# Performance work log

Hardware: AMD Instinct MI355X
Metric: run time of the kernel (lower is better)

Reference implementation:

```python
import jax, jax.numpy as jnp
import numpy as np

EMBED_DIM = 768
SCALE = float(np.sqrt(EMBED_DIM / 9.0))


def setup_inputs() -> dict:
    key = jax.random.key(0)
    ks = jax.random.split(key, 7)
    D = EMBED_DIM
    s = 1.0 / np.sqrt(D)
    x = jax.random.normal(ks[0], (8, 2048, D), dtype=jnp.float32)
    Wq = jax.random.uniform(ks[1], (D, D), jnp.float32, -s, s)
    bq = jax.random.uniform(ks[2], (D,), jnp.float32, -s, s)
    Wk = jax.random.uniform(ks[3], (D, D), jnp.float32, -s, s)
    bk = jax.random.uniform(ks[4], (D,), jnp.float32, -s, s)
    Wv = jax.random.uniform(ks[5], (D, D), jnp.float32, -s, s)
    bv = jax.random.uniform(ks[6], (D,), jnp.float32, -s, s)
    return {"x": x, "Wq": Wq, "bq": bq, "Wk": Wk, "bk": bk, "Wv": Wv, "bv": bv}


def reference(x, Wq, bq, Wk, bk, Wv, bv):
    # nn.Linear: y = x @ W^T + b
    Q = jnp.einsum('bnd,ed->bne', x, Wq) + bq
    K = jnp.einsum('bnd,ed->bne', x, Wk) + bk
    V = jnp.einsum('bnd,ed->bne', x, Wv) + bv
    scores = jnp.einsum('bqd,bkd->bqk', Q, K) / SCALE  # [B, Nq, Nk]
    # NOTE: softmax over the QUERY axis (dim=-2), per the original module
    weights = jax.nn.softmax(scores, axis=-2)
    out = jnp.einsum('bqk,bkd->bqd', weights, V)
    return out + x
```

## Files before the change

### kernel.cpp

```cpp
#include <hip/hip_runtime.h>
#include <stdint.h>

#define B_ 8
#define N_ 2048
#define D_ 768

typedef unsigned short u16;
typedef unsigned int u32;
typedef __attribute__((ext_vector_type(8))) short bf16x8;
typedef __attribute__((ext_vector_type(8))) unsigned short u16x8;
typedef __attribute__((ext_vector_type(4))) float f32x4;

static constexpr float INV_SCALE = 0.10825317547305482f;

__device__ __forceinline__ u16 f2bf(float f) {
  union { float f; unsigned u; } v; v.f = f;
  return (u16)((v.u + 0x7FFFu + ((v.u >> 16) & 1u)) >> 16);
}
__device__ __forceinline__ float bf2f(u16 h) {
  union { unsigned u; float f; } v; v.u = ((unsigned)h) << 16;
  return v.f;
}
__device__ __forceinline__ f32x4 mfma16(bf16x8 a, bf16x8 b, f32x4 c) {
  return __builtin_amdgcn_mfma_f32_16x16x32_bf16(a, b, c, 0, 0, 0);
}
__device__ __forceinline__ void gl_lds16(const u16* g, u16* l) {
  __builtin_amdgcn_global_load_lds(
      (const __attribute__((address_space(1))) u32*)g,
      (__attribute__((address_space(3))) u32*)l, 16, 0, 0);
}

__global__ __launch_bounds__(256) void cast_kernel(
    const float* __restrict__ x, const float* __restrict__ wq,
    const float* __restrict__ wk, const float* __restrict__ wv,
    u16* __restrict__ xb, u16* __restrict__ wqb,
    u16* __restrict__ wkb, u16* __restrict__ wvb) {
  const long NX = (long)B_ * N_ * D_;
  const long NW = (long)D_ * D_;
  long i = ((long)blockIdx.x * 256 + threadIdx.x) * 8;
  const float* src; u16* dst; long off;
  if (i < NX) { src = x; dst = xb; off = i; }
  else {
    long j = i - NX;
    int seg = (int)(j / NW);
    off = j - (long)seg * NW;
    src = seg == 0 ? wq : (seg == 1 ? wk : wv);
    dst = seg == 0 ? wqb : (seg == 1 ? wkb : wvb);
  }
  float4 a = *(const float4*)(src + off);
  float4 b = *(const float4*)(src + off + 4);
  u16x8 o;
  o[0]=f2bf(a.x); o[1]=f2bf(a.y); o[2]=f2bf(a.z); o[3]=f2bf(a.w);
  o[4]=f2bf(b.x); o[5]=f2bf(b.y); o[6]=f2bf(b.z); o[7]=f2bf(b.w);
  *(u16x8*)(dst + off) = o;
}

template<int KSTEPS>
__device__ __forceinline__ void gemm_main(
    const u16* __restrict__ Ag, long lda,
    const u16* __restrict__ Bg, long ldb,
    f32x4 (&acc)[8][4]) {
  __shared__ u16 A0[4096], A1[4096], A2[4096];
  __shared__ u16 B0[8192], B1[8192], B2[8192];
  const int t_ = threadIdx.x, l = t_ & 63, w = t_ >> 6;
  const int lr = l & 15;
  const int srow = l >> 2;
  const int scol = (((l & 3) ^ ((l >> 3) & 3)) * 8);
  const int wc = w * 64;
  const int rslot = (((l >> 4) ^ ((lr >> 1) & 3)) * 8);

  auto STAGE = [&](u16* As, u16* Bs, int kt) {
    const int kofs = kt * 32;
    #pragma unroll
    for (int c = 0; c < 6; ++c) {
      int ch = w * 6 + c;
      if (ch < 8)
        gl_lds16(Ag + (long)(ch * 16 + srow) * lda + kofs + scol, As + ch * 512);
      else
        gl_lds16(Bg + (long)((ch - 8) * 16 + srow) * ldb + kofs + scol,
                 Bs + (ch - 8) * 512);
    }
  };

#define PH(AS, BS, VM, DOSTAGE, ST)                                \
  {                                                                \
    asm volatile("s_waitcnt vmcnt(" #VM ")" ::: "memory");         \
    __builtin_amdgcn_s_barrier();                                  \
    asm volatile("" ::: "memory");                                 \
    bf16x8 a[8], bb[4];                                            \
    _Pragma("unroll")                                              \
    for (int mf = 0; mf < 8; ++mf)                                 \
      a[mf] = *(const bf16x8*)(AS + (mf * 16 + lr) * 32 + rslot);  \
    _Pragma("unroll")                                              \
    for (int nf = 0; nf < 4; ++nf)                                 \
      bb[nf] = *(const bf16x8*)(BS + (wc + nf * 16 + lr) * 32 + rslot); \
    __builtin_amdgcn_s_setprio(1);                                 \
    _Pragma("unroll")                                              \
    for (int mf = 0; mf < 8; ++mf)                                 \
      _Pragma("unroll")                                            \
      for (int nf = 0; nf < 4; ++nf)                               \
        acc[mf][nf] = mfma16(a[mf], bb[nf], acc[mf][nf]);          \
    __builtin_amdgcn_s_setprio(0);                                 \
    asm volatile("" ::: "memory");                                 \
    __builtin_amdgcn_s_barrier();                                  \
    if (DOSTAGE) STAGE(AS, BS, ST);                                \
  }

  STAGE(A0, B0, 0);
  STAGE(A1, B1, 1);
  STAGE(A2, B2, 2);
  int t = 0;
  for (; t + 5 < KSTEPS; t += 3) {
    PH(A0, B0, 12, true, t + 3);
    PH(A1, B1, 12, true, t + 4);
    PH(A2, B2, 12, true, t + 5);
  }
  if constexpr (KSTEPS % 3 == 1) {
    PH(A0, B0, 12, true, t + 3);
    PH(A1, B1, 12, false, 0);
    PH(A2, B2, 6, false, 0);
    PH(A0, B0, 0, false, 0);
  } else {
    PH(A0, B0, 12, false, 0);
    PH(A1, B1, 6, false, 0);
    PH(A2, B2, 0, false, 0);
  }
#undef PH
}

__global__ __launch_bounds__(256, 2) void qkv_gemm(
    const u16* __restrict__ xb,
    const u16* __restrict__ wq, const u16* __restrict__ wk, const u16* __restrict__ wv,
    const float* __restrict__ bq, const float* __restrict__ bk, const float* __restrict__ bv,
    u16* __restrict__ Qs, u16* __restrict__ Kb, u16* __restrict__ Vb) {
  const int lin = blockIdx.x;
  const int xcd = lin & 7, inner = lin >> 3;
  const int rt = xcd * 16 + (inner & 15);
  const int rest = inner >> 4;
  const int ct = rest % 3, mat = rest / 3;
  const u16* W = mat == 0 ? wq : (mat == 1 ? wk : wv);
  const float* bias = mat == 0 ? bq : (mat == 1 ? bk : bv);
  u16* out = mat == 0 ? Qs : (mat == 1 ? Kb : Vb);
  const float scl = mat == 0 ? INV_SCALE : 1.0f;
  const int rbase = rt * 128, cbase = ct * 256;

  f32x4 acc[8][4] = {};
  gemm_main<D_ / 32>(xb + (long)rbase * D_, D_, W + (long)cbase * D_, D_, acc);

  const int l = threadIdx.x & 63, w = threadIdx.x >> 6;
  const int lr = l & 15, orow = (l >> 4) * 4, wc = w * 64;
  #pragma unroll
  for (int mf = 0; mf < 8; ++mf)
    #pragma unroll
    for (int nf = 0; nf < 4; ++nf) {
      int col = cbase + wc + nf * 16 + lr;
      float bc = bias[col];
      #pragma unroll
      for (int r = 0; r < 4; ++r) {
        int row = rbase + mf * 16 + orow + r;
        out[(long)row * D_ + col] = f2bf((acc[mf][nf][r] + bc) * scl);
      }
    }
}

__global__ __launch_bounds__(256, 2) void qk_exp(
    const u16* __restrict__ Qs, const u16* __restrict__ Kb,
    u16* __restrict__ P, float* __restrict__ denpart) {
  const int lin = blockIdx.x;
  const int L = (lin & 7) * 128 + (lin >> 3);
  const int kblk = L % 8, qblk = (L / 8) % 16, b = L / 128;

  f32x4 acc[8][4] = {};
  gemm_main<D_ / 32>(Qs + ((long)b * N_ + qblk * 128) * D_, D_,
                     Kb + ((long)b * N_ + kblk * 256) * D_, D_, acc);

  const int tt = threadIdx.x, l = tt & 63, w = tt >> 6;
  const int lr = l & 15, orow = (l >> 4) * 4, wc = w * 64;
  float csum[4] = {0.f, 0.f, 0.f, 0.f};
  #pragma unroll
  for (int mf = 0; mf < 8; ++mf)
    #pragma unroll
    for (int nf = 0; nf < 4; ++nf) {
      long kk = kblk * 256 + wc + nf * 16 + lr;
      #pragma unroll
      for (int r = 0; r < 4; ++r) {
        long q = qblk * 128 + mf * 16 + orow + r;
        float e = __expf(acc[mf][nf][r]);
        u16 pe = f2bf(e);
        P[((long)b * N_ + q) * N_ + kk] = pe;
        csum[nf] += bf2f(pe);
      }
    }
  #pragma unroll
  for (int nf = 0; nf < 4; ++nf) {
    csum[nf] += __shfl_xor(csum[nf], 16);
    csum[nf] += __shfl_xor(csum[nf], 32);
  }
  if (l < 16) {
    #pragma unroll
    for (int nf = 0; nf < 4; ++nf)
      denpart[((long)qblk * B_ + b) * N_ + kblk * 256 + wc + nf * 16 + l] = csum[nf];
  }
}

__global__ __launch_bounds__(256) void scale_transpose(
    const u16* __restrict__ Vb, const float* __restrict__ denpart,
    u16* __restrict__ VsT) {
  const int b = blockIdx.z, k0 = blockIdx.y * 64, d0 = blockIdx.x * 64;
  __shared__ float tile[64][65];
  __shared__ float invden[64];
  const int t = threadIdx.x;
  if (t < 64) {
    float s = 0.f;
    for (int qs = 0; qs < 16; ++qs)
      s += denpart[((long)qs * B_ + b) * N_ + k0 + t];
    invden[t] = 1.0f / s;
  }
  __syncthreads();
  for (int idx = t; idx < 4096; idx += 256) {
    int kl = idx >> 6, dl = idx & 63;
    float v = bf2f(Vb[((long)b * N_ + k0 + kl) * D_ + d0 + dl]) * invden[kl];
    tile[dl][kl] = v;
  }
  __syncthreads();
  for (int idx = t; idx < 4096; idx += 256) {
    int dl = idx >> 6, kl = idx & 63;
    VsT[((long)b * D_ + d0 + dl) * N_ + k0 + kl] = f2bf(tile[dl][kl]);
  }
}

__global__ __launch_bounds__(256, 2) void pv_gemm(
    const u16* __restrict__ P, const u16* __restrict__ VsT,
    const u16* __restrict__ xb, float* __restrict__ out) {
  const int lin = blockIdx.x;
  const int L = (lin & 7) * 48 + (lin >> 3);
  const int qt = L % 16, dt = (L / 16) % 3, b = L / 48;
  const int q0 = qt * 128, d0 = dt * 256;

  f32x4 acc[8][4] = {};
  gemm_main<N_ / 32>(P + ((long)b * N_ + q0) * N_, N_,
                     VsT + ((long)b * D_ + d0) * N_, N_, acc);

  const int l = threadIdx.x & 63, w = threadIdx.x >> 6;
  const int lr = l & 15, orow = (l >> 4) * 4, wc = w * 64;
  #pragma unroll
  for (int mf = 0; mf < 8; ++mf)
    #pragma unroll
    for (int nf = 0; nf < 4; ++nf) {
      int dd = d0 + wc + nf * 16 + lr;
      #pragma unroll
      for (int r = 0; r < 4; ++r) {
        int q = q0 + mf * 16 + orow + r;
        long idx = ((long)b * N_ + q) * D_ + dd;
        out[idx] = acc[mf][nf][r] + bf2f(xb[idx]);
      }
    }
}

extern "C" void kernel_launch(void* const* d_in, const int* in_sizes, int n_in,
                              void* d_out, int out_size, void* d_ws, size_t ws_size,
                              hipStream_t stream) {
  const float* x  = (const float*)d_in[0];
  const float* Wq = (const float*)d_in[1];
  const float* bq = (const float*)d_in[2];
  const float* Wk = (const float*)d_in[3];
  const float* bk = (const float*)d_in[4];
  const float* Wv = (const float*)d_in[5];
  const float* bv = (const float*)d_in[6];

  char* ws = (char*)d_ws;
  u16* xb  = (u16*)(ws + 0);
  u16* wqb = (u16*)(ws + 25165824);
  u16* wkb = (u16*)(ws + 26345472);
  u16* wvb = (u16*)(ws + 27525120);
  u16* Qs  = (u16*)(ws + 28704768);
  u16* Kb  = (u16*)(ws + 53870592);
  u16* Vb  = (u16*)(ws + 79036416);
  u16* VsT = (u16*)(ws + 104202240);
  u16* P   = (u16*)(ws + 129368064);
  float* denpart = (float*)(ws + 196476928);
  (void)in_sizes; (void)n_in; (void)out_size; (void)ws_size;

  cast_kernel<<<7008, 256, 0, stream>>>(x, Wq, Wk, Wv, xb, wqb, wkb, wvb);
  qkv_gemm<<<1152, 256, 0, stream>>>(xb, wqb, wkb, wvb, bq, bk, bv, Qs, Kb, Vb);
  qk_exp<<<1024, 256, 0, stream>>>(Qs, Kb, P, denpart);
  scale_transpose<<<dim3(12, 32, 8), 256, 0, stream>>>(Vb, denpart, VsT);
  pv_gemm<<<384, 256, 0, stream>>>(P, VsT, xb, (float*)d_out);
}
```

Before: 225.2 us.

## Switch GEMMs to 256x256 tiles with 8 waves, BK=64 double buffering

Replaces the 128x256 triple-buffered GEMM core with a 256x256 tile computed by 512 threads (2x4 wave grid), using a K-step of 64 with double-buffered LDS and an XOR swizzle. Each k-step is split into four quadrant phases with barriers between them. All three GEMM kernels (QKV projection, QK^T+exp, PV) adopt the larger tile, halving the grid sizes and changing the block-to-XCD mapping. The larger tile raises arithmetic intensity and cuts global traffic, but it uses 128KB of LDS per block and leaves far fewer blocks, which hurts occupancy and tail balance (pv_gemm only has 192 blocks).

Result: slower. 275.9 us (+22.5%).

```diff
diff --git a/kernel.cpp b/kernel.cpp
--- a/kernel.cpp
+++ b/kernel.cpp
@@ -55,136 +55,151 @@
   *(u16x8*)(dst + off) = o;
 }
 
-template<int KSTEPS>
-__device__ __forceinline__ void gemm_main(
+template<int NT>
+__device__ __forceinline__ void gemm256(
     const u16* __restrict__ Ag, long lda,
     const u16* __restrict__ Bg, long ldb,
     f32x4 (&acc)[8][4]) {
-  __shared__ u16 A0[4096], A1[4096], A2[4096];
-  __shared__ u16 B0[8192], B1[8192], B2[8192];
+  __shared__ u16 Ab[2][16384];
+  __shared__ u16 Bb[2][16384];
   const int t_ = threadIdx.x, l = t_ & 63, w = t_ >> 6;
-  const int lr = l & 15;
-  const int srow = l >> 2;
-  const int scol = (((l & 3) ^ ((l >> 3) & 3)) * 8);
-  const int wc = w * 64;
-  const int rslot = (((l >> 4) ^ ((lr >> 1) & 3)) * 8);
-
+  const int lr = l & 15, kq = l >> 4;
+  const int wm = w >> 2, wn = w & 3;
+  const int arow = wm * 128, brow = wn * 64;
+
+  const int s_rowl = l >> 3;
+  const int s_sl = (l & 7) ^ (l >> 3);
   auto STAGE = [&](u16* As, u16* Bs, int kt) {
-    const int kofs = kt * 32;
-    #pragma unroll
-    for (int c = 0; c < 6; ++c) {
-      int ch = w * 6 + c;
-      if (ch < 8)
-        gl_lds16(Ag + (long)(ch * 16 + srow) * lda + kofs + scol, As + ch * 512);
-      else
-        gl_lds16(Bg + (long)((ch - 8) * 16 + srow) * ldb + kofs + scol,
-                 Bs + (ch - 8) * 512);
+    #pragma unroll
+    for (int j = 0; j < 4; ++j) {
+      const int dofs = (j * 8192 + w * 1024) >> 1;
+      const int row = j * 64 + w * 8 + s_rowl;
+      gl_lds16(Ag + (long)row * lda + kt * 64 + s_sl * 8, As + dofs);
+      gl_lds16(Bg + (long)row * ldb + kt * 64 + s_sl * 8, Bs + dofs);
     }
   };
 
-#define PH(AS, BS, VM, DOSTAGE, ST)                                \
-  {                                                                \
-    asm volatile("s_waitcnt vmcnt(" #VM ")" ::: "memory");         \
-    __builtin_amdgcn_s_barrier();                                  \
-    asm volatile("" ::: "memory");                                 \
-    bf16x8 a[8], bb[4];                                            \
-    _Pragma("unroll")                                              \
-    for (int mf = 0; mf < 8; ++mf)                                 \
-      a[mf] = *(const bf16x8*)(AS + (mf * 16 + lr) * 32 + rslot);  \
-    _Pragma("unroll")                                              \
-    for (int nf = 0; nf < 4; ++nf)                                 \
-      bb[nf] = *(const bf16x8*)(BS + (wc + nf * 16 + lr) * 32 + rslot); \
-    __builtin_amdgcn_s_setprio(1);                                 \
-    _Pragma("unroll")                                              \
-    for (int mf = 0; mf < 8; ++mf)                                 \
-      _Pragma("unroll")                                            \
-      for (int nf = 0; nf < 4; ++nf)                               \
-        acc[mf][nf] = mfma16(a[mf], bb[nf], acc[mf][nf]);          \
-    __builtin_amdgcn_s_setprio(0);                                 \
-    asm volatile("" ::: "memory");                                 \
-    __builtin_amdgcn_s_barrier();                                  \
-    if (DOSTAGE) STAGE(AS, BS, ST);                                \
-  }
-
-  STAGE(A0, B0, 0);
-  STAGE(A1, B1, 1);
-  STAGE(A2, B2, 2);
-  int t = 0;
-  for (; t + 5 < KSTEPS; t += 3) {
-    PH(A0, B0, 12, true, t + 3);
-    PH(A1, B1, 12, true, t + 4);
-    PH(A2, B2, 12, true, t + 5);
-  }
-  if constexpr (KSTEPS % 3 == 1) {
-    PH(A0, B0, 12, true, t + 3);
-    PH(A1, B1, 12, false, 0);
-    PH(A2, B2, 6, false, 0);
-    PH(A0, B0, 0, false, 0);
-  } else {
-    PH(A0, B0, 12, false, 0);
-    PH(A1, B1, 6, false, 0);
-    PH(A2, B2, 0, false, 0);
-  }
-#undef PH
-}
-
-__global__ __launch_bounds__(256, 2) void qkv_gemm(
+#define PHQ(AS, BS, QM, QN)                                              \
+  {                                                                      \
+    bf16x8 af[4][2], bf[2][2];                                           \
+    _Pragma("unroll")                                                    \
+    for (int mf = 0; mf < 4; ++mf) {                                     \
+      const int row = arow + (QM * 4 + mf) * 16 + lr;                    \
+      _Pragma("unroll")                                                  \
+      for (int ks = 0; ks < 2; ++ks)                                     \
+        af[mf][ks] = *(const bf16x8*)(AS + row * 64 +                    \
+                        (((4 * ks + kq) ^ (lr & 7)) * 8));               \
+    }                                                                    \
+    _Pragma("unroll")                                                    \
+    for (int nf = 0; nf < 2; ++nf) {                                     \
+      const int row = brow + (QN * 2 + nf) * 16 + lr;                    \
+      _Pragma("unroll")                                                  \
+      for (int ks = 0; ks < 2; ++ks)                                     \
+        bf[nf][ks] = *(const bf16x8*)(BS + row * 64 +                    \
+                        (((4 * ks + kq) ^ (lr & 7)) * 8));               \
+    }                                                                    \
+    __builtin_amdgcn_s_barrier();                                        \
+    __builtin_amdgcn_s_setprio(1);                                       \
+    _Pragma("unroll")                                                    \
+    for (int mf = 0; mf < 4; ++mf)                                       \
+      _Pragma("unroll")                                                  \
+      for (int nf = 0; nf < 2; ++nf)                                     \
+        acc[QM * 4 + mf][QN * 2 + nf] =                                  \
+            mfma16(af[mf][0], bf[nf][0], acc[QM * 4 + mf][QN * 2 + nf]); \
+    _Pragma("unroll")                                                    \
+    for (int mf = 0; mf < 4; ++mf)                                       \
+      _Pragma("unroll")                                                  \
+      for (int nf = 0; nf < 2; ++nf)                                     \
+        acc[QM * 4 + mf][QN * 2 + nf] =                                  \
+            mfma16(af[mf][1], bf[nf][1], acc[QM * 4 + mf][QN * 2 + nf]); \
+    __builtin_amdgcn_s_setprio(0);                                       \
+    asm volatile("" ::: "memory");                                       \
+    __builtin_amdgcn_s_barrier();                                        \
+  }
+
+#define TILE(AC, BC, AN, BN2, kt, DOST)                                  \
+  {                                                                      \
+    if (DOST) {                                                          \
+      STAGE(AN, BN2, (kt) + 1);                                          \
+      asm volatile("s_waitcnt vmcnt(8)" ::: "memory");                   \
+    } else {                                                             \
+      asm volatile("s_waitcnt vmcnt(0)" ::: "memory");                   \
+    }                                                                    \
+    __builtin_amdgcn_s_barrier();                                        \
+    PHQ(AC, BC, 0, 0)                                                    \
+    PHQ(AC, BC, 0, 1)                                                    \
+    PHQ(AC, BC, 1, 0)                                                    \
+    PHQ(AC, BC, 1, 1)                                                    \
+  }
+
+  STAGE(Ab[0], Bb[0], 0);
+  for (int t2 = 0; t2 < NT; t2 += 2) {
+    TILE(Ab[0], Bb[0], Ab[1], Bb[1], t2, true)
+    TILE(Ab[1], Bb[1], Ab[0], Bb[0], t2 + 1, (t2 + 2 < NT))
+  }
+#undef TILE
+#undef PHQ
+}
+
+__global__ __launch_bounds__(512, 2) void qkv_gemm(
     const u16* __restrict__ xb,
     const u16* __restrict__ wq, const u16* __restrict__ wk, const u16* __restrict__ wv,
     const float* __restrict__ bq, const float* __restrict__ bk, const float* __restrict__ bv,
     u16* __restrict__ Qs, u16* __restrict__ Kb, u16* __restrict__ Vb) {
   const int lin = blockIdx.x;
   const int xcd = lin & 7, inner = lin >> 3;
-  const int rt = xcd * 16 + (inner & 15);
-  const int rest = inner >> 4;
+  const int rt = xcd * 8 + (inner & 7);
+  const int rest = inner >> 3;
   const int ct = rest % 3, mat = rest / 3;
   const u16* W = mat == 0 ? wq : (mat == 1 ? wk : wv);
   const float* bias = mat == 0 ? bq : (mat == 1 ? bk : bv);
   u16* out = mat == 0 ? Qs : (mat == 1 ? Kb : Vb);
   const float scl = mat == 0 ? INV_SCALE : 1.0f;
-  const int rbase = rt * 128, cbase = ct * 256;
+  const int rbase = rt * 256, cbase = ct * 256;
 
   f32x4 acc[8][4] = {};
-  gemm_main<D_ / 32>(xb + (long)rbase * D_, D_, W + (long)cbase * D_, D_, acc);
+  gemm256<D_ / 64>(xb + (long)rbase * D_, D_, W + (long)cbase * D_, D_, acc);
 
   const int l = threadIdx.x & 63, w = threadIdx.x >> 6;
-  const int lr = l & 15, orow = (l >> 4) * 4, wc = w * 64;
+  const int lr = l & 15, orow = (l >> 4) * 4;
+  const int wm = w >> 2, wn = w & 3;
   #pragma unroll
   for (int mf = 0; mf < 8; ++mf)
     #pragma unroll
     for (int nf = 0; nf < 4; ++nf) {
-      int col = cbase + wc + nf * 16 + lr;
+      int col = cbase + wn * 64 + nf * 16 + lr;
       float bc = bias[col];
       #pragma unroll
       for (int r = 0; r < 4; ++r) {
-        int row = rbase + mf * 16 + orow + r;
+        int row = rbase + wm * 128 + mf * 16 + orow + r;
         out[(long)row * D_ + col] = f2bf((acc[mf][nf][r] + bc) * scl);
       }
     }
 }
 
-__global__ __launch_bounds__(256, 2) void qk_exp(
+__global__ __launch_bounds__(512, 2) void qk_exp(
     const u16* __restrict__ Qs, const u16* __restrict__ Kb,
     u16* __restrict__ P, float* __restrict__ denpart) {
   const int lin = blockIdx.x;
-  const int L = (lin & 7) * 128 + (lin >> 3);
-  const int kblk = L % 8, qblk = (L / 8) % 16, b = L / 128;
+  const int b = lin & 7, inner = lin >> 3;
+  const int kblk = inner & 7, qblk = inner >> 3;
 
   f32x4 acc[8][4] = {};
-  gemm_main<D_ / 32>(Qs + ((long)b * N_ + qblk * 128) * D_, D_,
-                     Kb + ((long)b * N_ + kblk * 256) * D_, D_, acc);
+  gemm256<D_ / 64>(Qs + ((long)b * N_ + qblk * 256) * D_, D_,
+                   Kb + ((long)b * N_ + kblk * 256) * D_, D_, acc);
 
   const int tt = threadIdx.x, l = tt & 63, w = tt >> 6;
-  const int lr = l & 15, orow = (l >> 4) * 4, wc = w * 64;
+  const int lr = l & 15, orow = (l >> 4) * 4;
+  const int wm = w >> 2, wn = w & 3;
   float csum[4] = {0.f, 0.f, 0.f, 0.f};
   #pragma unroll
   for (int mf = 0; mf < 8; ++mf)
     #pragma unroll
     for (int nf = 0; nf < 4; ++nf) {
-      long kk = kblk * 256 + wc + nf * 16 + lr;
+      long kk = kblk * 256 + wn * 64 + nf * 16 + lr;
       #pragma unroll
       for (int r = 0; r < 4; ++r) {
-        long q = qblk * 128 + mf * 16 + orow + r;
+        long q = qblk * 256 + wm * 128 + mf * 16 + orow + r;
         float e = __expf(acc[mf][nf][r]);
         u16 pe = f2bf(e);
         P[((long)b * N_ + q) * N_ + kk] = pe;
@@ -199,7 +214,8 @@
   if (l < 16) {
     #pragma unroll
     for (int nf = 0; nf < 4; ++nf)
-      denpart[((long)qblk * B_ + b) * N_ + kblk * 256 + wc + nf * 16 + l] = csum[nf];
+      denpart[((long)(qblk * 2 + wm) * B_ + b) * N_ +
+              kblk * 256 + wn * 64 + nf * 16 + l] = csum[nf];
   }
 }
 
@@ -229,28 +245,29 @@
   }
 }
 
-__global__ __launch_bounds__(256, 2) void pv_gemm(
+__global__ __launch_bounds__(512, 2) void pv_gemm(
     const u16* __restrict__ P, const u16* __restrict__ VsT,
     const u16* __restrict__ xb, float* __restrict__ out) {
   const int lin = blockIdx.x;
-  const int L = (lin & 7) * 48 + (lin >> 3);
-  const int qt = L % 16, dt = (L / 16) % 3, b = L / 48;
-  const int q0 = qt * 128, d0 = dt * 256;
+  const int b = lin & 7, inner = lin >> 3;
+  const int qt = inner % 8, dt = inner / 8;
+  const int q0 = qt * 256, d0 = dt * 256;
 
   f32x4 acc[8][4] = {};
-  gemm_main<N_ / 32>(P + ((long)b * N_ + q0) * N_, N_,
-                     VsT + ((long)b * D_ + d0) * N_, N_, acc);
+  gemm256<N_ / 64>(P + ((long)b * N_ + q0) * N_, N_,
+                   VsT + ((long)b * D_ + d0) * N_, N_, acc);
 
   const int l = threadIdx.x & 63, w = threadIdx.x >> 6;
-  const int lr = l & 15, orow = (l >> 4) * 4, wc = w * 64;
+  const int lr = l & 15, orow = (l >> 4) * 4;
+  const int wm = w >> 2, wn = w & 3;
   #pragma unroll
   for (int mf = 0; mf < 8; ++mf)
     #pragma unroll
     for (int nf = 0; nf < 4; ++nf) {
-      int dd = d0 + wc + nf * 16 + lr;
+      int dd = d0 + wn * 64 + nf * 16 + lr;
       #pragma unroll
       for (int r = 0; r < 4; ++r) {
-        int q = q0 + mf * 16 + orow + r;
+        int q = q0 + wm * 128 + mf * 16 + orow + r;
         long idx = ((long)b * N_ + q) * D_ + dd;
         out[idx] = acc[mf][nf][r] + bf2f(xb[idx]);
       }
@@ -282,8 +299,8 @@
   (void)in_sizes; (void)n_in; (void)out_size; (void)ws_size;
 
   cast_kernel<<<7008, 256, 0, stream>>>(x, Wq, Wk, Wv, xb, wqb, wkb, wvb);
-  qkv_gemm<<<1152, 256, 0, stream>>>(xb, wqb, wkb, wvb, bq, bk, bv, Qs, Kb, Vb);
-  qk_exp<<<1024, 256, 0, stream>>>(Qs, Kb, P, denpart);
+  qkv_gemm<<<576, 512, 0, stream>>>(xb, wqb, wkb, wvb, bq, bk, bv, Qs, Kb, Vb);
+  qk_exp<<<512, 512, 0, stream>>>(Qs, Kb, P, denpart);
   scale_transpose<<<dim3(12, 32, 8), 256, 0, stream>>>(Vb, denpart, VsT);
-  pv_gemm<<<384, 256, 0, stream>>>(P, VsT, xb, (float*)d_out);
-}
+  pv_gemm<<<192, 512, 0, stream>>>(P, VsT, xb, (float*)d_out);
+}
```
